# Optimization experiments

Hardware: AMD Instinct MI355X
Metric: run time of the kernel (lower is better)

The kernel has to match this reference:

```python
import jax, jax.numpy as jnp
import numpy as np
from jax import lax

B, L, E, P, K, KS, H, T = 64, 512, 256, 64, 512, 3, 512, 53
V, MAXL = 50000, 512


def _span_idx(k):
    ks, kl = jax.random.split(k)
    starts = jax.random.randint(ks, (B,), 1, L - 9)
    spans = jax.random.randint(kl, (B,), 0, 8)
    return jnp.stack([starts, starts + spans], axis=1)  # [B,2], 1<=s<=e<L-1


def setup_inputs() -> dict:
    key = jax.random.key(0)
    ks = jax.random.split(key, 12)
    context = jax.random.randint(ks[0], (B, L), 0, V)
    subject_idx = _span_idx(ks[1])
    object_idx = _span_idx(ks[2])
    subject_dis = jax.random.randint(ks[3], (B, L), 0, 2 * MAXL)
    object_dis = jax.random.randint(ks[4], (B, L), 0, 2 * MAXL)
    embed_table = jax.random.normal(ks[5], (V, E), jnp.float32) * 0.02
    pos_table = jax.random.normal(ks[6], (2 * MAXL, P), jnp.float32) * 0.02
    Cin = 3 * E + 2 * P
    conv_w = jax.random.normal(ks[7], (K, Cin, KS), jnp.float32) * 0.02
    conv_b = jnp.zeros((K,), jnp.float32)
    lin1_w = jax.random.normal(ks[8], (H, K), jnp.float32) * 0.02
    lin1_b = jnp.zeros((H,), jnp.float32)
    lin2_w = jax.random.normal(ks[9], (T, 6 * E + H), jnp.float32) * 0.02
    lin2_b = jnp.zeros((T,), jnp.float32)
    return {"context": context, "subject_idx": subject_idx, "object_idx": object_idx,
            "subject_dis": subject_dis, "object_dis": object_dis,
            "embed_table": embed_table, "pos_table": pos_table,
            "conv_w": conv_w, "conv_b": conv_b,
            "lin1_w": lin1_w, "lin1_b": lin1_b, "lin2_w": lin2_w, "lin2_b": lin2_b}


def _entity_features(embed, idx):
    # embed: [B,L,E'], idx: [B,2] (start,end) inclusive span
    s, e = idx[:, 0], idx[:, 1]
    pos = jnp.arange(L)
    mask = (pos[None, :] >= s[:, None]) & (pos[None, :] <= e[:, None])  # [B,L]
    cnt = mask.sum(axis=1).astype(embed.dtype)[:, None]
    mean = jnp.einsum('ble,bl->be', embed, mask.astype(embed.dtype)) / cnt
    bidx = jnp.arange(embed.shape[0])
    left = embed[bidx, s - 1]                       # start>=1 always in data (torch: start>=0 branch)
    right_ok = (e + 1) < L
    right = jnp.where(right_ok[:, None], embed[bidx, jnp.clip(e + 1, 0, L - 1)], 0.0)
    return jnp.concatenate([mean, left, right], axis=1)  # [B,3E']


def reference(context, subject_idx, object_idx, subject_dis, object_dis,
              embed_table, pos_table, conv_w, conv_b,
              lin1_w, lin1_b, lin2_w, lin2_b):
    embed = embed_table[context]                    # [B,L,E]
    subj = _entity_features(embed, subject_idx)     # [B,3E]
    obj = _entity_features(embed, object_idx)       # [B,3E]

    # shift-and-concat window features (zero pad one step each side)
    epad = jnp.pad(embed, ((0, 0), (1, 1), (0, 0)))
    word = jnp.concatenate([epad[:, :-2], epad[:, 1:-1], epad[:, 2:]], axis=2)  # [B,L,3E]

    pos_feat = jnp.concatenate([pos_table[subject_dis], pos_table[object_dis]], axis=2)  # [B,L,2P]
    sent = jnp.concatenate([word, pos_feat], axis=2).transpose(0, 2, 1)  # [B,C,L]

    conv = lax.conv_general_dilated(sent, conv_w, window_strides=(1,),
                                    padding=[(KS // 2, KS // 2)],
                                    dimension_numbers=('NCH', 'OIH', 'NCH'))
    conv = conv + conv_b[None, :, None]             # [B,K,L]
    pooled = conv.max(axis=2)                       # global maxpool -> [B,K]
    sent_h = jnp.tanh(pooled @ lin1_w.T + lin1_b)   # [B,H]

    com = jnp.concatenate([subj, obj, sent_h], axis=1)  # [B,6E+H]
    scores = com @ lin2_w.T + lin2_b                # [B,T]; decode = argmax(scores, 1)
    return scores
```

## Files before the change

### kernel.cpp

```cpp
#include <hip/hip_runtime.h>
#include <hip/hip_bf16.h>
#include <stdint.h>

#define B_   64
#define L_   512
#define E_   256
#define P_   64
#define KOUT 512
#define KS_  3
#define H_   512
#define T_   53
#define CINW 2688
#define LE   516
#define LPP  514
#define COMW 2048

#define SEC_CW    0
#define SEC_EMBP  512
#define SEC_POSP  (SEC_EMBP + (B_ * LE / 4))
#define SEC_ENT   (SEC_POSP + (B_ * LPP / 4))
#define SEC_POOL  (SEC_ENT + 2 * B_)
#define SEC_END   (SEC_POOL + 32)

typedef __attribute__((ext_vector_type(8))) short bf16x8;
typedef __attribute__((ext_vector_type(4))) float f32x4;

__device__ __forceinline__ unsigned enc_f(float x) {
    unsigned u = __float_as_uint(x);
    return (u & 0x80000000u) ? ~u : (u | 0x80000000u);
}
__device__ __forceinline__ float dec_f(unsigned e) {
    return __uint_as_float((e & 0x80000000u) ? (e & 0x7fffffffu) : ~e);
}

__device__ __forceinline__ void cp16(const void* g, void* l) {
    __builtin_amdgcn_global_load_lds(
        (const __attribute__((address_space(1))) unsigned int*)g,
        (__attribute__((address_space(3))) unsigned int*)l,
        16, 0, 0);
}

__global__ void prep(const float* __restrict__ conv_w,
                     const int* __restrict__ context,
                     const int* __restrict__ sidx,
                     const int* __restrict__ oidx,
                     const int* __restrict__ sdis,
                     const int* __restrict__ odis,
                     const float* __restrict__ etab,
                     const float* __restrict__ ptab,
                     __hip_bfloat16* __restrict__ wce,
                     __hip_bfloat16* __restrict__ wcp,
                     __hip_bfloat16* __restrict__ wcorr,
                     __hip_bfloat16* __restrict__ embp,
                     __hip_bfloat16* __restrict__ posp,
                     float* __restrict__ com,
                     unsigned* __restrict__ pooled) {
    __shared__ float w[CINW];
    const int blk = blockIdx.x;
    const int tid = threadIdx.x;

    if (blk < SEC_EMBP) {
        int n = blk;
        const float* src = conv_w + (size_t)n * CINW;
        for (int i = tid; i < CINW; i += 256) w[i] = src[i];
        __syncthreads();
        for (int i = tid; i < 5 * E_; i += 256) {
            int d = i >> 8, c = i & 255;
            float s = 0.f;
#pragma unroll
            for (int tau = 0; tau <= 2; tau++) {
                int seg = d - tau;
                if (seg >= 0 && seg <= 2) s += w[(seg * 256 + c) * 3 + tau];
            }
            wce[((size_t)d * KOUT + n) * E_ + c] = __float2bfloat16(s);
        }
        for (int i = tid; i < 3 * 128; i += 256) {
            int tau = i >> 7, p = i & 127;
            wcp[((size_t)tau * KOUT + n) * 128 + p] = __float2bfloat16(w[(768 + p) * 3 + tau]);
        }
        for (int i = tid; i < 2 * E_; i += 256) {
            int which = i >> 8, c = i & 255;
            wcorr[((size_t)which * KOUT + n) * E_ + c] =
                __float2bfloat16(which ? w[c * 3 + 2] : w[(512 + c) * 3 + 0]);
        }
    } else if (blk < SEC_POSP) {
        int row = (blk - SEC_EMBP) * 4 + (tid >> 6);
        int lane = tid & 63;
        int b = row / LE, r = row % LE;
        __hip_bfloat16* out = embp + (size_t)row * E_;
        if (r < 2 || r >= LE - 2) {
            *(ushort4*)(out + lane * 4) = (ushort4){0, 0, 0, 0};
            return;
        }
        int token = context[b * L_ + (r - 2)];
        float4 v = *(const float4*)(etab + (size_t)token * E_ + lane * 4);
        union { __hip_bfloat16 h[4]; ushort4 u; } pk;
        pk.h[0] = __float2bfloat16(v.x); pk.h[1] = __float2bfloat16(v.y);
        pk.h[2] = __float2bfloat16(v.z); pk.h[3] = __float2bfloat16(v.w);
        *(ushort4*)(out + lane * 4) = pk.u;
    } else if (blk < SEC_ENT) {
        int row = (blk - SEC_POSP) * 4 + (tid >> 6);
        int lane = tid & 63;
        int b = row / LPP, r = row % LPP;
        __hip_bfloat16* out = posp + (size_t)row * 128;
        if (r < 1 || r >= LPP - 1) {
            *(unsigned*)(out + lane * 2) = 0u;
            return;
        }
        int l = r - 1;
        int which = lane >> 5;
        int i2 = (lane & 31) * 2;
        int t = which ? odis[b * L_ + l] : sdis[b * L_ + l];
        float2 v = *(const float2*)(ptab + (size_t)t * P_ + i2);
        union { __hip_bfloat16 h[2]; unsigned u; } pk;
        pk.h[0] = __float2bfloat16(v.x); pk.h[1] = __float2bfloat16(v.y);
        *(unsigned*)(out + which * 64 + i2) = pk.u;
    } else if (blk < SEC_POOL) {
        int idx = blk - SEC_ENT;
        int b = idx >> 1, which = idx & 1;
        const int* sp = which ? oidx : sidx;
        int s = sp[b * 2 + 0], e = sp[b * 2 + 1];
        const int* ctx = context + b * L_;
        float* outb = com + (size_t)b * COMW + which * 768;
        int d = tid;
        float sum = 0.f;
        for (int x = s; x <= e; ++x) sum += etab[(size_t)ctx[x] * E_ + d];
        outb[d] = sum / (float)(e - s + 1);
        outb[256 + d] = etab[(size_t)ctx[s - 1] * E_ + d];
        float r = 0.f;
        if (e + 1 < L_) r = etab[(size_t)ctx[e + 1] * E_ + d];
        outb[512 + d] = r;
    } else {
        int base = ((blk - SEC_POOL) * 256 + tid) * 4;
        *(uint4*)(pooled + base) = (uint4){0, 0, 0, 0};
    }
}

__global__ void corr_k(const int* __restrict__ ctx,
                       const float* __restrict__ etab,
                       const __hip_bfloat16* __restrict__ wcorr,
                       float* __restrict__ corr) {
    int wid = blockIdx.x * 4 + (threadIdx.x >> 6);
    int lane = threadIdx.x & 63;
    int n4    = wid & 127;
    int which = (wid >> 7) & 1;
    int b     = wid >> 8;
    int token = ctx[b * L_ + (which ? L_ - 1 : 0)];
    float4 ev = *(const float4*)(etab + (size_t)token * E_ + lane * 4);
#pragma unroll
    for (int k = 0; k < 4; k++) {
        int n = n4 * 4 + k;
        const __hip_bfloat16* wr = wcorr + ((size_t)which * KOUT + n) * E_ + lane * 4;
        float s = ev.x * __bfloat162float(wr[0]) + ev.y * __bfloat162float(wr[1])
                + ev.z * __bfloat162float(wr[2]) + ev.w * __bfloat162float(wr[3]);
#pragma unroll
        for (int off = 32; off > 0; off >>= 1) s += __shfl_down(s, off, 64);
        if (lane == 0) corr[(b * 2 + which) * KOUT + n] = s;
    }
}

__global__ void conv_gemm_pool(const __hip_bfloat16* __restrict__ embp,
                               const __hip_bfloat16* __restrict__ posp,
                               const __hip_bfloat16* __restrict__ wce,
                               const __hip_bfloat16* __restrict__ wcp,
                               const float* __restrict__ corr,
                               unsigned* __restrict__ pooled) {
    __shared__ __hip_bfloat16 sA[128 * 32];
    __shared__ __hip_bfloat16 sB[128 * 32];

    const int tid  = threadIdx.x;
    const int wave = tid >> 6;
    const int lane = tid & 63;
    const int mt = blockIdx.x;
    const int nt = blockIdx.y;
    const int b  = mt >> 2;
    const int l0 = (mt & 3) * 128;
    const int n0 = nt * 128;

    const int wr = (wave & 1) * 64;
    const int wc = (wave >> 1) * 64;
    const int m  = lane & 15;
    const int q  = lane >> 4;

    f32x4 acc[4][4];
#pragma unroll
    for (int i = 0; i < 4; i++)
#pragma unroll
        for (int j = 0; j < 4; j++) acc[i][j] = (f32x4){0.f, 0.f, 0.f, 0.f};

    const int rowA = tid >> 2;
    const int cswz = (((tid & 3) ^ ((tid >> 3) & 3))) * 16;
    const int rsw  = (q ^ ((m >> 1) & 3)) * 16;

    auto step = [&](const char* Ab, int AsB, const char* Bb, int BsB) {
        cp16(Ab + rowA * AsB + cswz, (char*)sA + tid * 16);
        cp16(Bb + rowA * BsB + cswz, (char*)sB + tid * 16);
        cp16(Ab + (rowA + 64) * AsB + cswz, (char*)sA + (tid + 256) * 16);
        cp16(Bb + (rowA + 64) * BsB + cswz, (char*)sB + (tid + 256) * 16);
        __syncthreads();
        bf16x8 af[4], bfr[4];
#pragma unroll
        for (int i = 0; i < 4; i++)
            af[i] = *(const bf16x8*)((const char*)sA + (wr + i * 16 + m) * 64 + rsw);
#pragma unroll
        for (int j = 0; j < 4; j++)
            bfr[j] = *(const bf16x8*)((const char*)sB + (wc + j * 16 + m) * 64 + rsw);
#pragma unroll
        for (int i = 0; i < 4; i++)
#pragma unroll
            for (int j = 0; j < 4; j++)
                acc[i][j] = __builtin_amdgcn_mfma_f32_16x16x32_bf16(
                    af[i], bfr[j], acc[i][j], 0, 0, 0);
        __syncthreads();
    };

    for (int t = 0; t < 5; t++) {
        const char* Abase = (const char*)(embp + (size_t)(b * LE + l0 + t) * E_);
        const char* Bbase = (const char*)(wce + (size_t)(t * KOUT + n0) * E_);
        for (int kc = 0; kc < E_; kc += 32)
            step(Abase + kc * 2, E_ * 2, Bbase + kc * 2, E_ * 2);
    }
    for (int t = 0; t < 3; t++) {
        const char* Abase = (const char*)(posp + (size_t)(b * LPP + l0 + t) * 128);
        const char* Bbase = (const char*)(wcp + (size_t)(t * KOUT + n0) * 128);
        for (int kc = 0; kc < 128; kc += 32)
            step(Abase + kc * 2, 256, Bbase + kc * 2, 256);
    }

    const float* corrb = corr + b * 2 * KOUT;
#pragma unroll
    for (int j = 0; j < 4; j++) {
        int col = n0 + wc + j * 16 + m;
        float mx = -3.4e38f;
#pragma unroll
        for (int i = 0; i < 4; i++)
#pragma unroll
            for (int r = 0; r < 4; r++) {
                float v = acc[i][j][r];
                int l = l0 + wr + i * 16 + q * 4 + r;
                if (l == 0)      v -= corrb[col];
                if (l == L_ - 1) v -= corrb[KOUT + col];
                mx = fmaxf(mx, v);
            }
        mx = fmaxf(mx, __shfl_xor(mx, 16, 64));
        mx = fmaxf(mx, __shfl_xor(mx, 32, 64));
        if (q == 0) atomicMax(&pooled[b * KOUT + col], enc_f(mx));
    }
}

__global__ void lin1_k(const unsigned* __restrict__ pooled,
                       const float* __restrict__ conv_b,
                       const float* __restrict__ lin1_w,
                       const float* __restrict__ lin1_b,
                       float* __restrict__ com) {
    int bid = blockIdx.x;
    int wave = threadIdx.x >> 6, lane = threadIdx.x & 63;
    int b = bid >> 7;
    int h = (bid & 127) * 4 + wave;
    const float* w = lin1_w + (size_t)h * KOUT;
    const unsigned* pb = pooled + b * KOUT;
    float s = 0.f;
#pragma unroll
    for (int i = 0; i < 8; i++) {
        int k = lane + 64 * i;
        s += (dec_f(pb[k]) + conv_b[k]) * w[k];
    }
#pragma unroll
    for (int off = 32; off > 0; off >>= 1) s += __shfl_down(s, off, 64);
    if (lane == 0) com[(size_t)b * COMW + 1536 + h] = tanhf(s + lin1_b[h]);
}

__global__ void lin2_k(const float* __restrict__ com,
                       const float* __restrict__ lin2_w,
                       const float* __restrict__ lin2_b,
                       float* __restrict__ out) {
    int b = blockIdx.x;
    int wave = threadIdx.x >> 6, lane = threadIdx.x & 63;
    int t = blockIdx.y * 4 + wave;
    if (t >= T_) return;
    const float* w = lin2_w + (size_t)t * COMW;
    const float* c = com + (size_t)b * COMW;
    float s = 0.f;
#pragma unroll
    for (int i = 0; i < 32; i++) {
        int k = lane + 64 * i;
        s += c[k] * w[k];
    }
#pragma unroll
    for (int off = 32; off > 0; off >>= 1) s += __shfl_down(s, off, 64);
    if (lane == 0) out[b * T_ + t] = s + lin2_b[t];
}

extern "C" void kernel_launch(void* const* d_in, const int* in_sizes, int n_in,
                              void* d_out, int out_size, void* d_ws, size_t ws_size,
                              hipStream_t stream) {
    const int*   context = (const int*)d_in[0];
    const int*   sidx    = (const int*)d_in[1];
    const int*   oidx    = (const int*)d_in[2];
    const int*   sdis    = (const int*)d_in[3];
    const int*   odis    = (const int*)d_in[4];
    const float* etab    = (const float*)d_in[5];
    const float* ptab    = (const float*)d_in[6];
    const float* conv_w  = (const float*)d_in[7];
    const float* conv_b  = (const float*)d_in[8];
    const float* lin1_w  = (const float*)d_in[9];
    const float* lin1_b  = (const float*)d_in[10];
    const float* lin2_w  = (const float*)d_in[11];
    const float* lin2_b  = (const float*)d_in[12];
    float* out = (float*)d_out;

    char* ws = (char*)d_ws;
    size_t off = 0;
    __hip_bfloat16* embp = (__hip_bfloat16*)(ws + off);
    off += (size_t)B_ * LE * E_ * 2;
    off = (off + 255) & ~(size_t)255;
    __hip_bfloat16* posp = (__hip_bfloat16*)(ws + off);
    off += (size_t)B_ * LPP * 128 * 2;
    off = (off + 255) & ~(size_t)255;
    __hip_bfloat16* wce = (__hip_bfloat16*)(ws + off);
    off += (size_t)5 * KOUT * E_ * 2;
    off = (off + 255) & ~(size_t)255;
    __hip_bfloat16* wcp = (__hip_bfloat16*)(ws + off);
    off += (size_t)3 * KOUT * 128 * 2;
    off = (off + 255) & ~(size_t)255;
    __hip_bfloat16* wcorr = (__hip_bfloat16*)(ws + off);
    off += (size_t)2 * KOUT * E_ * 2;
    off = (off + 255) & ~(size_t)255;
    float* corr = (float*)(ws + off);
    off += (size_t)B_ * 2 * KOUT * 4;
    off = (off + 255) & ~(size_t)255;
    unsigned* pooled = (unsigned*)(ws + off);
    off += (size_t)B_ * KOUT * 4;
    off = (off + 255) & ~(size_t)255;
    float* com = (float*)(ws + off);
    off += (size_t)B_ * COMW * 4;

    prep<<<dim3(SEC_END), dim3(256), 0, stream>>>(
        conv_w, context, sidx, oidx, sdis, odis, etab, ptab,
        wce, wcp, wcorr, embp, posp, com, pooled);
    corr_k<<<dim3(4096), dim3(256), 0, stream>>>(context, etab, wcorr, corr);
    conv_gemm_pool<<<dim3(256, 4), dim3(256), 0, stream>>>(embp, posp, wce, wcp, corr, pooled);
    lin1_k<<<dim3(8192), dim3(256), 0, stream>>>(pooled, conv_b, lin1_w, lin1_b, com);
    lin2_k<<<dim3(B_, 14), dim3(256), 0, stream>>>(com, lin2_w, lin2_b, out);
}
```

Before: 214.1 us.

## Reuse shifted A tile across conv taps within each K chunk

Restructures the conv GEMM loop so each K chunk loads one A tile of 132 (or 130) rows plus the B tiles for all taps into shared memory at once. The taps then read shifted row windows of that single A tile. This replaces per-tap reloads of A and cuts the number of barriers from 48 to 12 per block. In exchange, shared memory grows to about 52 KB and the row-dependent swizzle on the A reads becomes more complex, which may lower occupancy.

```diff
diff --git a/kernel.cpp b/kernel.cpp
--- a/kernel.cpp
+++ b/kernel.cpp
@@ -165,8 +165,8 @@
                                const __hip_bfloat16* __restrict__ wcp,
                                const float* __restrict__ corr,
                                unsigned* __restrict__ pooled) {
-    __shared__ __hip_bfloat16 sA[128 * 32];
-    __shared__ __hip_bfloat16 sB[128 * 32];
+    __shared__ __hip_bfloat16 sA[768 * 8];
+    __shared__ __hip_bfloat16 sB[2560 * 8];
 
     const int tid  = threadIdx.x;
     const int wave = tid >> 6;
@@ -181,6 +181,7 @@
     const int wc = (wave >> 1) * 64;
     const int m  = lane & 15;
     const int q  = lane >> 4;
+    const int bsw = (q ^ ((m >> 1) & 3)) * 16;
 
     f32x4 acc[4][4];
 #pragma unroll
@@ -188,43 +189,82 @@
 #pragma unroll
         for (int j = 0; j < 4; j++) acc[i][j] = (f32x4){0.f, 0.f, 0.f, 0.f};
 
-    const int rowA = tid >> 2;
-    const int cswz = (((tid & 3) ^ ((tid >> 3) & 3))) * 16;
-    const int rsw  = (q ^ ((m >> 1) & 3)) * 16;
-
-    auto step = [&](const char* Ab, int AsB, const char* Bb, int BsB) {
-        cp16(Ab + rowA * AsB + cswz, (char*)sA + tid * 16);
-        cp16(Bb + rowA * BsB + cswz, (char*)sB + tid * 16);
-        cp16(Ab + (rowA + 64) * AsB + cswz, (char*)sA + (tid + 256) * 16);
-        cp16(Bb + (rowA + 64) * BsB + cswz, (char*)sB + (tid + 256) * 16);
-        __syncthreads();
-        bf16x8 af[4], bfr[4];
-#pragma unroll
-        for (int i = 0; i < 4; i++)
-            af[i] = *(const bf16x8*)((const char*)sA + (wr + i * 16 + m) * 64 + rsw);
-#pragma unroll
-        for (int j = 0; j < 4; j++)
-            bfr[j] = *(const bf16x8*)((const char*)sB + (wc + j * 16 + m) * 64 + rsw);
-#pragma unroll
-        for (int i = 0; i < 4; i++)
+    for (int kc = 0; kc < E_; kc += 32) {
+#pragma unroll
+        for (int r = 0; r < 3; r++) {
+            int s = r * 256 + tid;
+            int row = s >> 2; if (row > 131) row = 131;
+            int c = (s & 3) ^ ((row >> 1) & 3);
+            const char* src = (const char*)(embp + (size_t)(b * LE + l0 + row) * E_ + kc) + c * 16;
+            cp16(src, (char*)sA + s * 16);
+        }
+#pragma unroll
+        for (int r = 0; r < 10; r++) {
+            int s = r * 256 + tid;
+            int tap = s >> 9;
+            int n = (s >> 2) & 127;
+            int c = (s & 3) ^ ((n >> 1) & 3);
+            const char* src = (const char*)(wce + (size_t)(tap * KOUT + n0 + n) * E_ + kc) + c * 16;
+            cp16(src, (char*)sB + s * 16);
+        }
+        __syncthreads();
+#pragma unroll
+        for (int t = 0; t < 5; t++) {
+            const int asw = (q ^ (((m + t) >> 1) & 3)) * 16;
+            bf16x8 af[4], bfr[4];
+#pragma unroll
+            for (int i = 0; i < 4; i++)
+                af[i] = *(const bf16x8*)((const char*)sA + (wr + i * 16 + m + t) * 64 + asw);
 #pragma unroll
             for (int j = 0; j < 4; j++)
-                acc[i][j] = __builtin_amdgcn_mfma_f32_16x16x32_bf16(
-                    af[i], bfr[j], acc[i][j], 0, 0, 0);
-        __syncthreads();
-    };
-
-    for (int t = 0; t < 5; t++) {
-        const char* Abase = (const char*)(embp + (size_t)(b * LE + l0 + t) * E_);
-        const char* Bbase = (const char*)(wce + (size_t)(t * KOUT + n0) * E_);
-        for (int kc = 0; kc < E_; kc += 32)
-            step(Abase + kc * 2, E_ * 2, Bbase + kc * 2, E_ * 2);
-    }
-    for (int t = 0; t < 3; t++) {
-        const char* Abase = (const char*)(posp + (size_t)(b * LPP + l0 + t) * 128);
-        const char* Bbase = (const char*)(wcp + (size_t)(t * KOUT + n0) * 128);
-        for (int kc = 0; kc < 128; kc += 32)
-            step(Abase + kc * 2, 256, Bbase + kc * 2, 256);
+                bfr[j] = *(const bf16x8*)((const char*)sB + (t * 128 + wc + j * 16 + m) * 64 + bsw);
+#pragma unroll
+            for (int i = 0; i < 4; i++)
+#pragma unroll
+                for (int j = 0; j < 4; j++)
+                    acc[i][j] = __builtin_amdgcn_mfma_f32_16x16x32_bf16(
+                        af[i], bfr[j], acc[i][j], 0, 0, 0);
+        }
+        __syncthreads();
+    }
+
+    for (int kc = 0; kc < 128; kc += 32) {
+#pragma unroll
+        for (int r = 0; r < 3; r++) {
+            int s = r * 256 + tid;
+            int row = s >> 2; if (row > 129) row = 129;
+            int c = (s & 3) ^ ((row >> 1) & 3);
+            const char* src = (const char*)(posp + (size_t)(b * LPP + l0 + row) * 128 + kc) + c * 16;
+            cp16(src, (char*)sA + s * 16);
+        }
+#pragma unroll
+        for (int r = 0; r < 6; r++) {
+            int s = r * 256 + tid;
+            int tap = s >> 9;
+            int n = (s >> 2) & 127;
+            int c = (s & 3) ^ ((n >> 1) & 3);
+            const char* src = (const char*)(wcp + (size_t)(tap * KOUT + n0 + n) * 128 + kc) + c * 16;
+            cp16(src, (char*)sB + s * 16);
+        }
+        __syncthreads();
+#pragma unroll
+        for (int t = 0; t < 3; t++) {
+            const int asw = (q ^ (((m + t) >> 1) & 3)) * 16;
+            bf16x8 af[4], bfr[4];
+#pragma unroll
+            for (int i = 0; i < 4; i++)
+                af[i] = *(const bf16x8*)((const char*)sA + (wr + i * 16 + m + t) * 64 + asw);
+#pragma unroll
+            for (int j = 0; j < 4; j++)
+                bfr[j] = *(const bf16x8*)((const char*)sB + (t * 128 + wc + j * 16 + m) * 64 + bsw);
+#pragma unroll
+            for (int i = 0; i < 4; i++)
+#pragma unroll
+                for (int j = 0; j < 4; j++)
+                    acc[i][j] = __builtin_amdgcn_mfma_f32_16x16x32_bf16(
+                        af[i], bfr[j], acc[i][j], 0, 0, 0);
+        }
+        __syncthreads();
     }
 
     const float* corrb = corr + b * 2 * KOUT;
```

Result: no change. 213.0 us (-0.5%).

## Switch conv GEMM operands from bf16 to scaled fp8 e4m3 MFMA

Applied to the files above, without the earlier changes.

Quantizes embeddings, positional features and the folded conv weights to fp8 e4m3 with a fixed scale of 64, and runs the conv GEMM with fp8 MFMA instructions over 64-wide K chunks, descaling when pooling. This halves operand bytes in memory and LDS and uses the higher-throughput fp8 matrix path. The cost is reduced precision, since small values scaled by 64 may still underflow or lose accuracy in e4m3, which risks exceeding the output tolerance.

```diff
diff --git a/kernel.cpp b/kernel.cpp
--- a/kernel.cpp
+++ b/kernel.cpp
@@ -1,5 +1,6 @@
 #include <hip/hip_runtime.h>
 #include <hip/hip_bf16.h>
+#include <hip/hip_fp8.h>
 #include <stdint.h>
 
 #define B_   64
@@ -15,6 +16,9 @@
 #define LPP  514
 #define COMW 2048
 
+#define FP8_S    64.0f
+#define DESCALE  (1.0f / 4096.0f)
+
 #define SEC_CW    0
 #define SEC_EMBP  512
 #define SEC_POSP  (SEC_EMBP + (B_ * LE / 4))
@@ -22,7 +26,6 @@
 #define SEC_POOL  (SEC_ENT + 2 * B_)
 #define SEC_END   (SEC_POOL + 32)
 
-typedef __attribute__((ext_vector_type(8))) short bf16x8;
 typedef __attribute__((ext_vector_type(4))) float f32x4;
 
 __device__ __forceinline__ unsigned enc_f(float x) {
@@ -31,6 +34,10 @@
 }
 __device__ __forceinline__ float dec_f(unsigned e) {
     return __uint_as_float((e & 0x80000000u) ? (e & 0x7fffffffu) : ~e);
+}
+__device__ __forceinline__ unsigned char f8c(float x) {
+    __hip_fp8_e4m3 t(x);
+    return t.__x;
 }
 
 __device__ __forceinline__ void cp16(const void* g, void* l) {
@@ -48,11 +55,11 @@
                      const int* __restrict__ odis,
                      const float* __restrict__ etab,
                      const float* __restrict__ ptab,
-                     __hip_bfloat16* __restrict__ wce,
-                     __hip_bfloat16* __restrict__ wcp,
+                     unsigned char* __restrict__ wce,
+                     unsigned char* __restrict__ wcp,
                      __hip_bfloat16* __restrict__ wcorr,
-                     __hip_bfloat16* __restrict__ embp,
-                     __hip_bfloat16* __restrict__ posp,
+                     unsigned char* __restrict__ embp,
+                     unsigned char* __restrict__ posp,
                      float* __restrict__ com,
                      unsigned* __restrict__ pooled) {
     __shared__ float w[CINW];
@@ -72,11 +79,11 @@
                 int seg = d - tau;
                 if (seg >= 0 && seg <= 2) s += w[(seg * 256 + c) * 3 + tau];
             }
-            wce[((size_t)d * KOUT + n) * E_ + c] = __float2bfloat16(s);
+            wce[((size_t)d * KOUT + n) * E_ + c] = f8c(s * FP8_S);
         }
         for (int i = tid; i < 3 * 128; i += 256) {
             int tau = i >> 7, p = i & 127;
-            wcp[((size_t)tau * KOUT + n) * 128 + p] = __float2bfloat16(w[(768 + p) * 3 + tau]);
+            wcp[((size_t)tau * KOUT + n) * 128 + p] = f8c(w[(768 + p) * 3 + tau] * FP8_S);
         }
         for (int i = tid; i < 2 * E_; i += 256) {
             int which = i >> 8, c = i & 255;
@@ -87,24 +94,24 @@
         int row = (blk - SEC_EMBP) * 4 + (tid >> 6);
         int lane = tid & 63;
         int b = row / LE, r = row % LE;
-        __hip_bfloat16* out = embp + (size_t)row * E_;
+        unsigned char* out = embp + (size_t)row * E_;
         if (r < 2 || r >= LE - 2) {
-            *(ushort4*)(out + lane * 4) = (ushort4){0, 0, 0, 0};
+            *(uchar4*)(out + lane * 4) = (uchar4){0, 0, 0, 0};
             return;
         }
         int token = context[b * L_ + (r - 2)];
         float4 v = *(const float4*)(etab + (size_t)token * E_ + lane * 4);
-        union { __hip_bfloat16 h[4]; ushort4 u; } pk;
-        pk.h[0] = __float2bfloat16(v.x); pk.h[1] = __float2bfloat16(v.y);
-        pk.h[2] = __float2bfloat16(v.z); pk.h[3] = __float2bfloat16(v.w);
-        *(ushort4*)(out + lane * 4) = pk.u;
+        uchar4 pk;
+        pk.x = f8c(v.x * FP8_S); pk.y = f8c(v.y * FP8_S);
+        pk.z = f8c(v.z * FP8_S); pk.w = f8c(v.w * FP8_S);
+        *(uchar4*)(out + lane * 4) = pk;
     } else if (blk < SEC_ENT) {
         int row = (blk - SEC_POSP) * 4 + (tid >> 6);
         int lane = tid & 63;
         int b = row / LPP, r = row % LPP;
-        __hip_bfloat16* out = posp + (size_t)row * 128;
+        unsigned char* out = posp + (size_t)row * 128;
         if (r < 1 || r >= LPP - 1) {
-            *(unsigned*)(out + lane * 2) = 0u;
+            *(unsigned short*)(out + lane * 2) = 0;
             return;
         }
         int l = r - 1;
@@ -112,9 +119,9 @@
         int i2 = (lane & 31) * 2;
         int t = which ? odis[b * L_ + l] : sdis[b * L_ + l];
         float2 v = *(const float2*)(ptab + (size_t)t * P_ + i2);
-        union { __hip_bfloat16 h[2]; unsigned u; } pk;
-        pk.h[0] = __float2bfloat16(v.x); pk.h[1] = __float2bfloat16(v.y);
-        *(unsigned*)(out + which * 64 + i2) = pk.u;
+        unsigned short pk = (unsigned short)f8c(v.x * FP8_S)
+                          | ((unsigned short)f8c(v.y * FP8_S) << 8);
+        *(unsigned short*)(out + which * 64 + i2) = pk;
     } else if (blk < SEC_POOL) {
         int idx = blk - SEC_ENT;
         int b = idx >> 1, which = idx & 1;
@@ -159,14 +166,14 @@
     }
 }
 
-__global__ void conv_gemm_pool(const __hip_bfloat16* __restrict__ embp,
-                               const __hip_bfloat16* __restrict__ posp,
-                               const __hip_bfloat16* __restrict__ wce,
-                               const __hip_bfloat16* __restrict__ wcp,
+__global__ void conv_gemm_pool(const unsigned char* __restrict__ embp,
+                               const unsigned char* __restrict__ posp,
+                               const unsigned char* __restrict__ wce,
+                               const unsigned char* __restrict__ wcp,
                                const float* __restrict__ corr,
                                unsigned* __restrict__ pooled) {
-    __shared__ __hip_bfloat16 sA[128 * 32];
-    __shared__ __hip_bfloat16 sB[128 * 32];
+    __shared__ unsigned char sA[128 * 64];
+    __shared__ unsigned char sB[128 * 64];
 
     const int tid  = threadIdx.x;
     const int wave = tid >> 6;
@@ -189,8 +196,7 @@
         for (int j = 0; j < 4; j++) acc[i][j] = (f32x4){0.f, 0.f, 0.f, 0.f};
 
     const int rowA = tid >> 2;
-    const int cswz = (((tid & 3) ^ ((tid >> 3) & 3))) * 16;
-    const int rsw  = (q ^ ((m >> 1) & 3)) * 16;
+    const int cswz = ((tid & 3) ^ ((tid >> 3) & 3)) * 16;
 
     auto step = [&](const char* Ab, int AsB, const char* Bb, int BsB) {
         cp16(Ab + rowA * AsB + cswz, (char*)sA + tid * 16);
@@ -198,33 +204,42 @@
         cp16(Ab + (rowA + 64) * AsB + cswz, (char*)sA + (tid + 256) * 16);
         cp16(Bb + (rowA + 64) * BsB + cswz, (char*)sB + (tid + 256) * 16);
         __syncthreads();
-        bf16x8 af[4], bfr[4];
-#pragma unroll
-        for (int i = 0; i < 4; i++)
-            af[i] = *(const bf16x8*)((const char*)sA + (wr + i * 16 + m) * 64 + rsw);
-#pragma unroll
-        for (int j = 0; j < 4; j++)
-            bfr[j] = *(const bf16x8*)((const char*)sB + (wc + j * 16 + m) * 64 + rsw);
-#pragma unroll
-        for (int i = 0; i < 4; i++)
-#pragma unroll
-            for (int j = 0; j < 4; j++)
-                acc[i][j] = __builtin_amdgcn_mfma_f32_16x16x32_bf16(
-                    af[i], bfr[j], acc[i][j], 0, 0, 0);
+#pragma unroll
+        for (int h = 0; h < 2; h++) {
+            long af[4], bfr[4];
+#pragma unroll
+            for (int i = 0; i < 4; i++) {
+                int row = wr + i * 16 + m;
+                int pc = ((h << 1) | (q >> 1)) ^ ((row >> 1) & 3);
+                af[i] = *(const long*)((const char*)sA + row * 64 + pc * 16 + (q & 1) * 8);
+            }
+#pragma unroll
+            for (int j = 0; j < 4; j++) {
+                int row = wc + j * 16 + m;
+                int pc = ((h << 1) | (q >> 1)) ^ ((row >> 1) & 3);
+                bfr[j] = *(const long*)((const char*)sB + row * 64 + pc * 16 + (q & 1) * 8);
+            }
+#pragma unroll
+            for (int i = 0; i < 4; i++)
+#pragma unroll
+                for (int j = 0; j < 4; j++)
+                    acc[i][j] = __builtin_amdgcn_mfma_f32_16x16x32_fp8_fp8(
+                        af[i], bfr[j], acc[i][j], 0, 0, 0);
+        }
         __syncthreads();
     };
 
     for (int t = 0; t < 5; t++) {
         const char* Abase = (const char*)(embp + (size_t)(b * LE + l0 + t) * E_);
         const char* Bbase = (const char*)(wce + (size_t)(t * KOUT + n0) * E_);
-        for (int kc = 0; kc < E_; kc += 32)
-            step(Abase + kc * 2, E_ * 2, Bbase + kc * 2, E_ * 2);
+        for (int kc = 0; kc < E_; kc += 64)
+            step(Abase + kc, E_, Bbase + kc, E_);
     }
     for (int t = 0; t < 3; t++) {
         const char* Abase = (const char*)(posp + (size_t)(b * LPP + l0 + t) * 128);
         const char* Bbase = (const char*)(wcp + (size_t)(t * KOUT + n0) * 128);
-        for (int kc = 0; kc < 128; kc += 32)
-            step(Abase + kc * 2, 256, Bbase + kc * 2, 256);
+        for (int kc = 0; kc < 128; kc += 64)
+            step(Abase + kc, 128, Bbase + kc, 128);
     }
 
     const float* corrb = corr + b * 2 * KOUT;
@@ -236,7 +251,7 @@
         for (int i = 0; i < 4; i++)
 #pragma unroll
             for (int r = 0; r < 4; r++) {
-                float v = acc[i][j][r];
+                float v = acc[i][j][r] * DESCALE;
                 int l = l0 + wr + i * 16 + q * 4 + r;
                 if (l == 0)      v -= corrb[col];
                 if (l == L_ - 1) v -= corrb[KOUT + col];
@@ -311,17 +326,17 @@
 
     char* ws = (char*)d_ws;
     size_t off = 0;
-    __hip_bfloat16* embp = (__hip_bfloat16*)(ws + off);
-    off += (size_t)B_ * LE * E_ * 2;
-    off = (off + 255) & ~(size_t)255;
-    __hip_bfloat16* posp = (__hip_bfloat16*)(ws + off);
-    off += (size_t)B_ * LPP * 128 * 2;
-    off = (off + 255) & ~(size_t)255;
-    __hip_bfloat16* wce = (__hip_bfloat16*)(ws + off);
-    off += (size_t)5 * KOUT * E_ * 2;
-    off = (off + 255) & ~(size_t)255;
-    __hip_bfloat16* wcp = (__hip_bfloat16*)(ws + off);
-    off += (size_t)3 * KOUT * 128 * 2;
+    unsigned char* embp = (unsigned char*)(ws + off);
+    off += (size_t)B_ * LE * E_;
+    off = (off + 255) & ~(size_t)255;
+    unsigned char* posp = (unsigned char*)(ws + off);
+    off += (size_t)B_ * LPP * 128;
+    off = (off + 255) & ~(size_t)255;
+    unsigned char* wce = (unsigned char*)(ws + off);
+    off += (size_t)5 * KOUT * E_;
+    off = (off + 255) & ~(size_t)255;
+    unsigned char* wcp = (unsigned char*)(ws + off);
+    off += (size_t)3 * KOUT * 128;
     off = (off + 255) & ~(size_t)255;
     __hip_bfloat16* wcorr = (__hip_bfloat16*)(ws + off);
     off += (size_t)2 * KOUT * E_ * 2;
```

Result: faster. 189.4 us (median of 2 runs) (-11.6%).
